# Performance work log

Measured on AMD Instinct MI355X. Metric: run time of the kernel, lower is better.

## Reference

```python
import jax, jax.numpy as jnp
import numpy as np


def conv1x1(x, w, b):
    # x: [B,C,H,W], w: [O,C], b: [O] -> [B,O,H,W]
    return jnp.einsum('bchw,oc->bohw', x, w) + b[None, :, None, None]


def setup_inputs() -> dict:
    key = jax.random.key(0)
    ks = jax.random.split(key, 8)
    B, H, W = 32, 64, 64
    PoI_N, PT_feat, T_feat = 128, 64, 32
    poi = jax.random.uniform(ks[0], (B, PoI_N, H, W), dtype=jnp.float32)
    time = jax.random.normal(ks[1], (B, 31, H, W), dtype=jnp.float32)
    s = 0.05
    wm = jax.random.normal(ks[2], (T_feat, 31), dtype=jnp.float32) * s
    bm = jnp.zeros((T_feat,), jnp.float32)
    wf = jax.random.normal(ks[3], (1, T_feat), dtype=jnp.float32) * s
    bf = jnp.zeros((1,), jnp.float32)
    wc = jax.random.normal(ks[4], (PT_feat, PoI_N), dtype=jnp.float32) * s
    bc = jnp.zeros((PT_feat,), jnp.float32)
    return {'poi': poi, 'time': time, 'wm': wm, 'bm': bm, 'wf': wf, 'bf': bf, 'wc': wc, 'bc': bc}


def reference(poi, time, wm, bm, wf, bf, wc, bc):
    # Time_trans: conv1x1 -> relu -> conv1x1 -> relu, out channels = 1
    z = jax.nn.relu(conv1x1(time, wm, bm))
    T_x = jax.nn.relu(conv1x1(z, wf, bf))  # [B,1,H,W]
    # original does a detached CPU tile/multiply: broadcast multiply, no grad through it
    poi_time = jax.lax.stop_gradient(T_x * poi)  # [B,PoI_N,H,W]
    return conv1x1(poi_time, wc, bc)
```

## Files before the change

kernel.cpp:

```cpp
#include <hip/hip_runtime.h>
#include <hip/hip_bf16.h>

typedef short bf16x8 __attribute__((ext_vector_type(8)));
typedef float f32x4  __attribute__((ext_vector_type(4)));

constexpr int HW = 4096;
constexpr int CT = 31;
constexpr int CP = 128;
constexpr int CO = 64;

__device__ __forceinline__ short f2bf(float x) {
    __hip_bfloat16 h = __float2bfloat16(x);
    return *reinterpret_cast<short*>(&h);
}

__device__ __forceinline__ float async_load(const float* p) {
    float v;
    asm volatile("global_load_dword %0, %1, off" : "=v"(v) : "v"(p));
    return v;
}
#define VM_WAIT(n) asm volatile("s_waitcnt vmcnt(" #n ")" ::: "memory")
#define SBAR() __builtin_amdgcn_sched_barrier(0)

__global__ __launch_bounds__(256)
void poi_mfma7(const float* __restrict__ poi,
               const float* __restrict__ tin,
               const float* __restrict__ wm,
               const float* __restrict__ bm,
               const float* __restrict__ wf,
               const float* __restrict__ bf,
               const float* __restrict__ wc,
               const float* __restrict__ bc,
               float* __restrict__ out)
{
    const int lane = threadIdx.x & 63;
    const int m    = lane & 15;
    const int g    = lane >> 4;
    const int wid  = threadIdx.x >> 6;
    const int oh   = (wid & 1) * 2;
    const int b    = blockIdx.x >> 6;
    const int px0  = ((blockIdx.x & 63) << 6) + (wid >> 1) * 32;

    bf16x8 wcf[2][4];
    #pragma unroll
    for (int s = 0; s < 2; ++s)
      #pragma unroll
      for (int kf = 0; kf < 4; ++kf)
        #pragma unroll
        for (int j = 0; j < 8; ++j)
          wcf[s][kf][j] = f2bf(wc[((oh + s) * 16 + m) * CP + kf * 32 + g * 8 + j]);

    bf16x8 wmf[2];
    #pragma unroll
    for (int t2 = 0; t2 < 2; ++t2)
      #pragma unroll
      for (int j = 0; j < 8; ++j) {
        const int c = g * 8 + j;
        wmf[t2][j] = (c < CT) ? f2bf(wm[(t2 * 16 + m) * CT + c]) : (short)0;
      }
    float wff[8]; f32x4 bmf[2]; float bcf[2];
    #pragma unroll
    for (int t2 = 0; t2 < 2; ++t2)
      #pragma unroll
      for (int r = 0; r < 4; ++r) {
        wff[t2 * 4 + r] = wf[t2 * 16 + g * 4 + r];
        bmf[t2][r]      = bm[t2 * 16 + g * 4 + r];
      }
    #pragma unroll
    for (int s = 0; s < 2; ++s) bcf[s] = bc[(oh + s) * 16 + m];
    const float bfv = bf[0];

    const float* tbase = tin + (size_t)b * CT * HW;
    const float* pbase = poi + (size_t)b * CP * HW;
    float*       obase = out + (size_t)b * CO * HW;

    #pragma unroll
    for (int t = 0; t < 2; ++t) {
        const int pxt = px0 + t * 16;
        const float* tb = tbase + pxt + m;
        const float* pb = pbase + pxt + m;

        float tfr[8];
        #pragma unroll
        for (int j = 0; j < 8; ++j) {
            const int c  = g * 8 + j;
            const int cc = (c < CT) ? c : (CT - 1);
            tfr[j] = async_load(tb + (size_t)cc * HW);
        }
        float pfr[32];
        #pragma unroll
        for (int kf = 0; kf < 4; ++kf)
          #pragma unroll
          for (int j = 0; j < 8; ++j)
            pfr[kf * 8 + j] = async_load(pb + (size_t)(kf * 32 + g * 8 + j) * HW);
        SBAR();
        VM_WAIT(32);
        SBAR();

        bf16x8 tf;
        #pragma unroll
        for (int j = 0; j < 8; ++j) {
            const int c = g * 8 + j;
            tf[j] = (c < CT) ? f2bf(tfr[j]) : (short)0;
        }
        f32x4 z0 = __builtin_amdgcn_mfma_f32_16x16x32_bf16(wmf[0], tf, bmf[0], 0, 0, 0);
        f32x4 z1 = __builtin_amdgcn_mfma_f32_16x16x32_bf16(wmf[1], tf, bmf[1], 0, 0, 0);
        float s1 = 0.f;
        #pragma unroll
        for (int r = 0; r < 4; ++r) {
            s1 = fmaf(fmaxf(z0[r], 0.f), wff[r],     s1);
            s1 = fmaf(fmaxf(z1[r], 0.f), wff[4 + r], s1);
        }
        s1 += __shfl_xor(s1, 16, 64);
        s1 += __shfl_xor(s1, 32, 64);
        const float tval = fmaxf(s1 + bfv, 0.f);
        f32x4 tv;
        #pragma unroll
        for (int r = 0; r < 4; ++r) tv[r] = __shfl(tval, g * 4 + r, 64);

        SBAR();
        VM_WAIT(0);
        SBAR();

        bf16x8 pfv[4];
        #pragma unroll
        for (int kf = 0; kf < 4; ++kf)
          #pragma unroll
          for (int j = 0; j < 8; ++j)
            pfv[kf][j] = f2bf(pfr[kf * 8 + j]);

        float* ob = obase + pxt + g * 4;
        #pragma unroll
        for (int s = 0; s < 2; ++s) {
            f32x4 a = {0.f, 0.f, 0.f, 0.f};
            #pragma unroll
            for (int kf = 0; kf < 4; ++kf)
                a = __builtin_amdgcn_mfma_f32_16x16x32_bf16(pfv[kf], wcf[s][kf], a, 0, 0, 0);
            f32x4 v;
            #pragma unroll
            for (int r = 0; r < 4; ++r) v[r] = fmaf(tv[r], a[r], bcf[s]);
            __builtin_nontemporal_store(
                v, reinterpret_cast<f32x4*>(ob + (size_t)((oh + s) * 16 + m) * HW));
        }
    }
}

extern "C" void kernel_launch(void* const* d_in, const int* in_sizes, int n_in,
                              void* d_out, int out_size, void* d_ws, size_t ws_size,
                              hipStream_t stream) {
    const float* poi = (const float*)d_in[0];
    const float* tin = (const float*)d_in[1];
    const float* wm  = (const float*)d_in[2];
    const float* bm  = (const float*)d_in[3];
    const float* wf  = (const float*)d_in[4];
    const float* bf  = (const float*)d_in[5];
    const float* wc  = (const float*)d_in[6];
    const float* bc  = (const float*)d_in[7];
    float* out = (float*)d_out;

    hipLaunchKernelGGL(poi_mfma7, dim3(2048), dim3(256), 0, stream,
                       poi, tin, wm, bm, wf, bf, wc, bc, out);
}
```

Before: 38.39 us.

## Load two adjacent pixels per lane with dwordx2 and issue all loads at once

Replaces the two sequential 16-pixel iterations with one pass in which each lane loads two adjacent pixels using 8-byte global_load_dwordx2, so all of the wave's memory requests go out up front instead of in two phases. The MFMA work is duplicated for the even and odd pixel sets. Because the interleaved pixel order no longer matches the MFMA output layout, cross-lane shuffles rebuild contiguous 16-byte rows before the nontemporal stores. This adds shuffle work and roughly doubles the registers held for loaded data, which may reduce occupancy.

```diff
diff --git a/kernel.cpp b/kernel.cpp
--- a/kernel.cpp
+++ b/kernel.cpp
@@ -3,6 +3,7 @@
 
 typedef short bf16x8 __attribute__((ext_vector_type(8)));
 typedef float f32x4  __attribute__((ext_vector_type(4)));
+typedef float f32x2  __attribute__((ext_vector_type(2)));
 
 constexpr int HW = 4096;
 constexpr int CT = 31;
@@ -13,17 +14,16 @@
     __hip_bfloat16 h = __float2bfloat16(x);
     return *reinterpret_cast<short*>(&h);
 }
-
-__device__ __forceinline__ float async_load(const float* p) {
-    float v;
-    asm volatile("global_load_dword %0, %1, off" : "=v"(v) : "v"(p));
+__device__ __forceinline__ f32x2 async_load2(const float* p) {
+    f32x2 v;
+    asm volatile("global_load_dwordx2 %0, %1, off" : "=v"(v) : "v"(p));
     return v;
 }
 #define VM_WAIT(n) asm volatile("s_waitcnt vmcnt(" #n ")" ::: "memory")
 #define SBAR() __builtin_amdgcn_sched_barrier(0)
 
 __global__ __launch_bounds__(256)
-void poi_mfma7(const float* __restrict__ poi,
+void poi_mfma8(const float* __restrict__ poi,
                const float* __restrict__ tin,
                const float* __restrict__ wm,
                const float* __restrict__ bm,
@@ -70,78 +70,106 @@
     for (int s = 0; s < 2; ++s) bcf[s] = bc[(oh + s) * 16 + m];
     const float bfv = bf[0];
 
-    const float* tbase = tin + (size_t)b * CT * HW;
-    const float* pbase = poi + (size_t)b * CP * HW;
-    float*       obase = out + (size_t)b * CO * HW;
+    const float* tb = tin + (size_t)b * CT * HW + px0 + 2 * m;
+    const float* pb = poi + (size_t)b * CP * HW + px0 + 2 * m;
 
+    SBAR(); VM_WAIT(0); SBAR();
+
+    f32x2 tfr[8];
     #pragma unroll
-    for (int t = 0; t < 2; ++t) {
-        const int pxt = px0 + t * 16;
-        const float* tb = tbase + pxt + m;
-        const float* pb = pbase + pxt + m;
+    for (int j = 0; j < 8; ++j) {
+        const int c  = g * 8 + j;
+        const int cc = (c < CT) ? c : (CT - 1);
+        tfr[j] = async_load2(tb + (size_t)cc * HW);
+    }
+    f32x2 pfr[32];
+    #pragma unroll
+    for (int kf = 0; kf < 4; ++kf)
+      #pragma unroll
+      for (int j = 0; j < 8; ++j)
+        pfr[kf * 8 + j] = async_load2(pb + (size_t)(kf * 32 + g * 8 + j) * HW);
+    SBAR();
+    VM_WAIT(32);
+    SBAR();
 
-        float tfr[8];
+    bf16x8 tf0, tf1;
+    #pragma unroll
+    for (int j = 0; j < 8; ++j) {
+        const int c = g * 8 + j;
+        tf0[j] = (c < CT) ? f2bf(tfr[j][0]) : (short)0;
+        tf1[j] = (c < CT) ? f2bf(tfr[j][1]) : (short)0;
+    }
+    f32x4 z0x = __builtin_amdgcn_mfma_f32_16x16x32_bf16(wmf[0], tf0, bmf[0], 0, 0, 0);
+    f32x4 z1x = __builtin_amdgcn_mfma_f32_16x16x32_bf16(wmf[1], tf0, bmf[1], 0, 0, 0);
+    f32x4 z0y = __builtin_amdgcn_mfma_f32_16x16x32_bf16(wmf[0], tf1, bmf[0], 0, 0, 0);
+    f32x4 z1y = __builtin_amdgcn_mfma_f32_16x16x32_bf16(wmf[1], tf1, bmf[1], 0, 0, 0);
+    float sx = 0.f, sy = 0.f;
+    #pragma unroll
+    for (int r = 0; r < 4; ++r) {
+        sx = fmaf(fmaxf(z0x[r], 0.f), wff[r],     sx);
+        sx = fmaf(fmaxf(z1x[r], 0.f), wff[4 + r], sx);
+        sy = fmaf(fmaxf(z0y[r], 0.f), wff[r],     sy);
+        sy = fmaf(fmaxf(z1y[r], 0.f), wff[4 + r], sy);
+    }
+    sx += __shfl_xor(sx, 16, 64);  sx += __shfl_xor(sx, 32, 64);
+    sy += __shfl_xor(sy, 16, 64);  sy += __shfl_xor(sy, 32, 64);
+    const float tval0 = fmaxf(sx + bfv, 0.f);
+    const float tval1 = fmaxf(sy + bfv, 0.f);
+    f32x4 tv0, tv1;
+    #pragma unroll
+    for (int r = 0; r < 4; ++r) {
+        tv0[r] = __shfl(tval0, g * 4 + r, 64);
+        tv1[r] = __shfl(tval1, g * 4 + r, 64);
+    }
+
+    SBAR();
+    VM_WAIT(0);
+    SBAR();
+
+    bf16x8 pf0[4], pf1[4];
+    #pragma unroll
+    for (int kf = 0; kf < 4; ++kf)
+      #pragma unroll
+      for (int j = 0; j < 8; ++j) {
+        pf0[kf][j] = f2bf(pfr[kf * 8 + j][0]);
+        pf1[kf][j] = f2bf(pfr[kf * 8 + j][1]);
+      }
+    f32x4 a0[2], a1[2];
+    #pragma unroll
+    for (int s = 0; s < 2; ++s) { a0[s] = f32x4{0.f,0.f,0.f,0.f}; a1[s] = f32x4{0.f,0.f,0.f,0.f}; }
+    #pragma unroll
+    for (int kf = 0; kf < 4; ++kf) {
         #pragma unroll
-        for (int j = 0; j < 8; ++j) {
-            const int c  = g * 8 + j;
-            const int cc = (c < CT) ? c : (CT - 1);
-            tfr[j] = async_load(tb + (size_t)cc * HW);
+        for (int s = 0; s < 2; ++s) {
+            a0[s] = __builtin_amdgcn_mfma_f32_16x16x32_bf16(pf0[kf], wcf[s][kf], a0[s], 0, 0, 0);
+            a1[s] = __builtin_amdgcn_mfma_f32_16x16x32_bf16(pf1[kf], wcf[s][kf], a1[s], 0, 0, 0);
         }
-        float pfr[32];
-        #pragma unroll
-        for (int kf = 0; kf < 4; ++kf)
-          #pragma unroll
-          for (int j = 0; j < 8; ++j)
-            pfr[kf * 8 + j] = async_load(pb + (size_t)(kf * 32 + g * 8 + j) * HW);
-        SBAR();
-        VM_WAIT(32);
-        SBAR();
+    }
 
-        bf16x8 tf;
-        #pragma unroll
-        for (int j = 0; j < 8; ++j) {
-            const int c = g * 8 + j;
-            tf[j] = (c < CT) ? f2bf(tfr[j]) : (short)0;
-        }
-        f32x4 z0 = __builtin_amdgcn_mfma_f32_16x16x32_bf16(wmf[0], tf, bmf[0], 0, 0, 0);
-        f32x4 z1 = __builtin_amdgcn_mfma_f32_16x16x32_bf16(wmf[1], tf, bmf[1], 0, 0, 0);
-        float s1 = 0.f;
+    const int srcA = ((g >> 1) << 4) + m;
+    const int srcB = srcA + 32;
+    #pragma unroll
+    for (int s = 0; s < 2; ++s) {
+        float v[8];
         #pragma unroll
         for (int r = 0; r < 4; ++r) {
-            s1 = fmaf(fmaxf(z0[r], 0.f), wff[r],     s1);
-            s1 = fmaf(fmaxf(z1[r], 0.f), wff[4 + r], s1);
+            v[2 * r]     = fmaf(tv0[r], a0[s][r], bcf[s]);
+            v[2 * r + 1] = fmaf(tv1[r], a1[s][r], bcf[s]);
         }
-        s1 += __shfl_xor(s1, 16, 64);
-        s1 += __shfl_xor(s1, 32, 64);
-        const float tval = fmaxf(s1 + bfv, 0.f);
-        f32x4 tv;
+        f32x4 lo, hi;
         #pragma unroll
-        for (int r = 0; r < 4; ++r) tv[r] = __shfl(tval, g * 4 + r, 64);
-
-        SBAR();
-        VM_WAIT(0);
-        SBAR();
-
-        bf16x8 pfv[4];
-        #pragma unroll
-        for (int kf = 0; kf < 4; ++kf)
-          #pragma unroll
-          for (int j = 0; j < 8; ++j)
-            pfv[kf][j] = f2bf(pfr[kf * 8 + j]);
-
-        float* ob = obase + pxt + g * 4;
-        #pragma unroll
-        for (int s = 0; s < 2; ++s) {
-            f32x4 a = {0.f, 0.f, 0.f, 0.f};
-            #pragma unroll
-            for (int kf = 0; kf < 4; ++kf)
-                a = __builtin_amdgcn_mfma_f32_16x16x32_bf16(pfv[kf], wcf[s][kf], a, 0, 0, 0);
-            f32x4 v;
-            #pragma unroll
-            for (int r = 0; r < 4; ++r) v[r] = fmaf(tv[r], a[r], bcf[s]);
-            __builtin_nontemporal_store(
-                v, reinterpret_cast<f32x4*>(ob + (size_t)((oh + s) * 16 + m) * HW));
+        for (int q = 0; q < 4; ++q) {
+            const float aA = __shfl(v[q], srcA, 64);
+            const float bA = __shfl(v[q + 4], srcA, 64);
+            lo[q] = (g & 1) ? bA : aA;
+            const float aB = __shfl(v[q], srcB, 64);
+            const float bB = __shfl(v[q + 4], srcB, 64);
+            hi[q] = (g & 1) ? bB : aB;
         }
+        float* orow = out + (size_t)b * CO * HW
+                          + (size_t)((oh + s) * 16 + m) * HW + px0;
+        __builtin_nontemporal_store(lo, reinterpret_cast<f32x4*>(orow + 4 * g));
+        __builtin_nontemporal_store(hi, reinterpret_cast<f32x4*>(orow + 16 + 4 * g));
     }
 }
 
@@ -158,6 +186,6 @@
     const float* bc  = (const float*)d_in[7];
     float* out = (float*)d_out;
 
-    hipLaunchKernelGGL(poi_mfma7, dim3(2048), dim3(256), 0, stream,
+    hipLaunchKernelGGL(poi_mfma8, dim3(2048), dim3(256), 0, stream,
                        poi, tin, wm, bm, wf, bf, wc, bc, out);
 }
```

New measurement: 39.24 us. 1.02x slower.
